# Kernel tuning notes

Hardware: AMD Instinct MI355X
Metric: run time of the kernel (lower is better)

The kernel has to match this reference:

```python
import jax, jax.numpy as jnp
import numpy as np

D = 1024
HS = 64
NH = D // HS


def setup_inputs() -> dict:
    key = jax.random.key(0)
    ks = jax.random.split(key, 8)
    B, S = 2, 2048
    x = jax.random.normal(ks[0], (B, S, D), dtype=jnp.float32)
    y = jax.random.normal(ks[1], (B, S, D), dtype=jnp.float32)
    pad_mask = jax.random.randint(ks[2], (B, S), 0, 2).astype(jnp.int32)
    sc = 1.0 / np.sqrt(D)
    Wq = jax.random.normal(ks[3], (D, D), dtype=jnp.float32) * sc
    Wk = jax.random.normal(ks[4], (D, D), dtype=jnp.float32) * sc
    Wv = jax.random.normal(ks[5], (D, D), dtype=jnp.float32) * sc
    Wp = jax.random.normal(ks[6], (D, D), dtype=jnp.float32) * sc
    bp = jnp.zeros((D,), dtype=jnp.float32)
    return {"x": x, "y": y, "pad_mask": pad_mask, "Wq": Wq, "Wk": Wk, "Wv": Wv, "Wp": Wp, "bp": bp}


def reference(x, y, pad_mask, Wq, Wk, Wv, Wp, bp):
    B, S, _ = x.shape
    # torch Linear: out = in @ W.T  (bias=False for q/k/v)
    q = (y @ Wq.T).reshape(B, S, NH, HS).transpose(0, 2, 1, 3)  # [B,H,S,hs]
    k = (x @ Wk.T).reshape(B, S, NH, HS).transpose(0, 2, 1, 3)
    v = (x @ Wv.T).reshape(B, S, NH, HS).transpose(0, 2, 1, 3)
    att = jnp.einsum('bhqd,bhkd->bhqk', q, k) * (HS ** -0.5)  # [B,H,S,S]
    att = jnp.where((pad_mask == 0)[:, None, None, :], -jnp.inf, att)
    att = jax.nn.softmax(att, axis=-1)
    out = jnp.einsum('bhqk,bhkd->bhqd', att, v)  # [B,H,S,hs]
    out = out.transpose(0, 2, 1, 3).reshape(B, S, D)
    return out @ Wp.T + bp
```

## Files before the change

kernel.cpp:

```cpp
#include <hip/hip_runtime.h>
#include <hip/hip_bf16.h>
#include <stdint.h>

typedef unsigned short u16;
typedef unsigned int u32;
typedef float __attribute__((ext_vector_type(4))) f32x4;
typedef __bf16 __attribute__((ext_vector_type(8))) bfrag;
typedef u16 __attribute__((ext_vector_type(8))) u16x8;

#define DEV static __device__ __forceinline__

DEV u16 f2bf(float f) {
  union { float f; u32 u; } c; c.f = f;
  u32 u = c.u;
  u += 0x7fffu + ((u >> 16) & 1u);
  return (u16)(u >> 16);
}

DEV u16 bf16bits(float f) {
  __hip_bfloat16 h = __float2bfloat16(f);
  return *reinterpret_cast<u16*>(&h);
}

DEV float exp2a(float x) { return __builtin_amdgcn_exp2f(x); }

typedef const u32 __attribute__((address_space(1)))* gas_t;
typedef u32 __attribute__((address_space(3)))* las_t;

DEV void async16(const void* g, void* l) {
  __builtin_amdgcn_global_load_lds((gas_t)(uintptr_t)g, (las_t)(uintptr_t)l, 16, 0, 0);
}

__global__ __launch_bounds__(256) void convert_all(
    const float* __restrict__ x, const float* __restrict__ y,
    const float* __restrict__ wq, const float* __restrict__ wk,
    const float* __restrict__ wv, const float* __restrict__ wp,
    u16* __restrict__ xb, u16* __restrict__ yb,
    u16* __restrict__ wqb, u16* __restrict__ wkb,
    u16* __restrict__ wvb, u16* __restrict__ wpb) {
  const int NX4 = (2 * 2048 * 1024) / 4;
  const int NW4 = (1024 * 1024) / 4;
  const int total = 2 * NX4 + 4 * NW4;
  for (int i = blockIdx.x * blockDim.x + threadIdx.x; i < total;
       i += gridDim.x * blockDim.x) {
    const float4* s; ushort4* d; int off;
    if (i < NX4) { s = (const float4*)x; d = (ushort4*)xb; off = i; }
    else if (i < 2 * NX4) { s = (const float4*)y; d = (ushort4*)yb; off = i - NX4; }
    else {
      int k = i - 2 * NX4; int wsel = k >> 18; off = k & (NW4 - 1);
      s = (const float4*)(wsel == 0 ? wq : wsel == 1 ? wk : wsel == 2 ? wv : wp);
      d = (ushort4*)(wsel == 0 ? wqb : wsel == 1 ? wkb : wsel == 2 ? wvb : wpb);
    }
    float4 v = s[off];
    ushort4 o; o.x = f2bf(v.x); o.y = f2bf(v.y); o.z = f2bf(v.z); o.w = f2bf(v.w);
    d[off] = o;
  }
}

__global__ __launch_bounds__(256, 3) void gemm_qkv(
    const u16* __restrict__ xb, const u16* __restrict__ yb,
    const u16* __restrict__ wqb, const u16* __restrict__ wkb,
    const u16* __restrict__ wvb,
    u16* __restrict__ Qb, u16* __restrict__ Kb2, u16* __restrict__ Vtb) {
  const int Kd = 1024, Nd = 1024;
  __shared__ __align__(16) u16 arena[18432];
  u16* Als = arena;
  u16* Bls = arena + 8192;

  const int gid = blockIdx.x;
  const int seg = gid >> 8;
  const int bb = gid & 255;
  const int m0 = (bb >> 3) * 128, n0 = (bb & 7) * 128;
  const u16* A  = (seg == 0) ? yb : xb;
  const u16* Bw = (seg == 0) ? wqb : (seg == 1 ? wkb : wvb);

  const int t = threadIdx.x;
  const int lane = t & 63, w = t >> 6;
  const int wr = w >> 1, wc = w & 1;
  const int r15 = lane & 15, g = lane >> 4;
  const int rdx = (r15 & 7) << 3;

  const int srow = t >> 3;
  const int scol = ((t & 7) ^ (srow & 7)) * 8;

  f32x4 acc[4][4] = {{}};
  const u16* ga = A + (size_t)(m0 + srow) * Kd + scol;
  const u16* gb = Bw + (size_t)(n0 + srow) * Kd + scol;

  for (int k0 = 0; k0 < Kd; k0 += 64) {
#pragma unroll
    for (int c = 0; c < 4; ++c) {
      async16(ga + (size_t)c * 32 * Kd + k0, &Als[c * 2048 + t * 8]);
      async16(gb + (size_t)c * 32 * Kd + k0, &Bls[c * 2048 + t * 8]);
    }
    __syncthreads();
#pragma unroll
    for (int ks = 0; ks < 2; ++ks) {
      const int cb = (ks * 32 + g * 8) ^ rdx;
      bfrag af[4], bfr[4];
#pragma unroll
      for (int i = 0; i < 4; i++)
        af[i] = *(const bfrag*)&Als[(wr * 64 + i * 16 + r15) * 64 + cb];
#pragma unroll
      for (int j = 0; j < 4; j++)
        bfr[j] = *(const bfrag*)&Bls[(wc * 64 + j * 16 + r15) * 64 + cb];
#pragma unroll
      for (int i = 0; i < 4; i++)
#pragma unroll
        for (int j = 0; j < 4; j++)
          acc[i][j] = __builtin_amdgcn_mfma_f32_16x16x32_bf16(af[i], bfr[j], acc[i][j], 0, 0, 0);
    }
    __syncthreads();
  }

  if (seg < 2) {
    u16* C = (seg == 0) ? Qb : Kb2;
    const float scale = (seg == 0) ? 0.18033688f : 1.0f;
#pragma unroll
    for (int i = 0; i < 4; i++) {
#pragma unroll
      for (int j = 0; j < 4; j++) {
        int col = n0 + wc * 64 + j * 16 + r15;
        int row = m0 + wr * 64 + i * 16 + g * 4;
#pragma unroll
        for (int r = 0; r < 4; r++)
          C[(size_t)(row + r) * Nd + col] = f2bf(acc[i][j][r] * scale);
      }
    }
  } else {
    u16* Tw = arena + w * 4608;
#pragma unroll
    for (int i = 0; i < 4; i++)
#pragma unroll
      for (int j = 0; j < 4; j++)
#pragma unroll
        for (int r = 0; r < 4; r++)
          Tw[(j * 16 + r15) * 72 + (i * 16 + g * 4 + r)] = f2bf(acc[i][j][r]);
#pragma unroll
    for (int it = 0; it < 8; ++it) {
      int slot = lane + it * 64;
      int nl = slot >> 3, sgm = slot & 7;
      int4 vrow = *(const int4*)&Tw[nl * 72 + sgm * 8];
      int col = n0 + wc * 64 + nl;
      int h = col >> 6, hs = col & 63;
      int rowg = m0 + wr * 64 + sgm * 8;
      int b = rowg >> 11, s = rowg & 2047;
      *(int4*)&Vtb[(((size_t)b * 16 + h) * 64 + hs) * 2048 + s] = vrow;
    }
  }
}

__global__ __launch_bounds__(256, 2) void gemm_proj(
    const u16* __restrict__ A, const u16* __restrict__ Bw,
    float* __restrict__ C, const float* __restrict__ bias) {
  const int Kd = 1024, Nd = 1024;
  __shared__ __align__(16) u16 Als[64 * 64];
  __shared__ __align__(16) u16 Bls[128 * 64];
  const int t = threadIdx.x;
  const int lane = t & 63, w = t >> 6;
  const int wr = w >> 1, wc = w & 1;
  const int r15 = lane & 15, g = lane >> 4;
  const int m0 = blockIdx.y * 64, n0 = blockIdx.x * 128;
  const int rdx = (r15 & 7) << 3;
  const int srow = t >> 3;
  const int scol = ((t & 7) ^ (srow & 7)) * 8;

  f32x4 acc[2][4] = {{}};
  const u16* ga = A + (size_t)(m0 + srow) * Kd + scol;
  const u16* gb = Bw + (size_t)(n0 + srow) * Kd + scol;

  for (int k0 = 0; k0 < Kd; k0 += 64) {
#pragma unroll
    for (int c = 0; c < 2; ++c)
      async16(ga + (size_t)c * 32 * Kd + k0, &Als[c * 2048 + t * 8]);
#pragma unroll
    for (int c = 0; c < 4; ++c)
      async16(gb + (size_t)c * 32 * Kd + k0, &Bls[c * 2048 + t * 8]);
    __syncthreads();
#pragma unroll
    for (int ks = 0; ks < 2; ++ks) {
      const int cb = (ks * 32 + g * 8) ^ rdx;
      bfrag af[2], bfr[4];
#pragma unroll
      for (int i = 0; i < 2; i++)
        af[i] = *(const bfrag*)&Als[(wr * 32 + i * 16 + r15) * 64 + cb];
#pragma unroll
      for (int j = 0; j < 4; j++)
        bfr[j] = *(const bfrag*)&Bls[(wc * 64 + j * 16 + r15) * 64 + cb];
#pragma unroll
      for (int i = 0; i < 2; i++)
#pragma unroll
        for (int j = 0; j < 4; j++)
          acc[i][j] = __builtin_amdgcn_mfma_f32_16x16x32_bf16(af[i], bfr[j], acc[i][j], 0, 0, 0);
    }
    __syncthreads();
  }

#pragma unroll
  for (int i = 0; i < 2; i++) {
#pragma unroll
    for (int j = 0; j < 4; j++) {
      int col = n0 + wc * 64 + j * 16 + r15;
      int row = m0 + wr * 32 + i * 16 + g * 4;
      float bv = bias[col];
#pragma unroll
      for (int r = 0; r < 4; r++)
        C[(size_t)(row + r) * Nd + col] = acc[i][j][r] + bv;
    }
  }
}

__global__ __launch_bounds__(256, 2) void attn_fwd(
    const u16* __restrict__ Q, const u16* __restrict__ Kb,
    const u16* __restrict__ Vt, const int* __restrict__ mask,
    u16* __restrict__ O) {
  __shared__ __align__(16) u16 Kls[2][64 * 64];
  __shared__ __align__(16) u16 Vls[2][64 * 64];
  __shared__ __align__(16) u16 Pls[4][32 * 64];
  __shared__ float biasl[2][64];

  const int bid = blockIdx.x;
  const int swz = (bid & 7) * 64 + (bid >> 3);
  const int qblk = swz & 15, bh = swz >> 4;
  const int b = bh >> 4, h = bh & 15;
  const int t = threadIdx.x, lane = t & 63, w = t >> 6;
  const int r15 = lane & 15, g = lane >> 4;
  const int qbase = qblk * 128 + w * 32;

  bfrag aQ[2][2];
  {
    const u16* Qg = Q + ((size_t)b * 2048 + qbase) * 1024 + h * 64;
#pragma unroll
    for (int mf = 0; mf < 2; ++mf)
#pragma unroll
      for (int ks = 0; ks < 2; ++ks)
        aQ[mf][ks] = *(const bfrag*)&Qg[(size_t)(mf * 16 + r15) * 1024 + ks * 32 + g * 8];
  }

  bfrag ones;
  {
    u16x8 ob = {0x3F80, 0x3F80, 0x3F80, 0x3F80, 0x3F80, 0x3F80, 0x3F80, 0x3F80};
    ones = *(bfrag*)&ob;
  }

  f32x4 oacc[2][4] = {};
  f32x4 osum[2] = {};

  const u16* Kg = Kb + (size_t)b * 2048 * 1024 + h * 64;
  const u16* Vg = Vt + (size_t)bh * 64 * 2048;
  const int* mg = mask + b * 2048;

  const int rdx = (r15 & 7) << 3;
  const int srow = t >> 3;
  const int scol = (((t & 7) ^ (srow & 7)) * 8);

  auto stage_async = [&](int kv0, int buf) {
    async16(&Kg[(size_t)(kv0 + srow) * 1024 + scol],        &Kls[buf][t * 8]);
    async16(&Kg[(size_t)(kv0 + 32 + srow) * 1024 + scol],   &Kls[buf][2048 + t * 8]);
    async16(&Vg[(size_t)srow * 2048 + kv0 + scol],          &Vls[buf][t * 8]);
    async16(&Vg[(size_t)(32 + srow) * 2048 + kv0 + scol],   &Vls[buf][2048 + t * 8]);
  };

  stage_async(0, 0);
  if (t < 64) biasl[0][t] = mg[t] ? 0.f : -1e30f;
  __syncthreads();

  float nbias = 0.f;
  for (int kt = 0; kt < 32; ++kt) {
    const int cur = kt & 1;
    if (kt < 31) {
      stage_async((kt + 1) * 64, cur ^ 1);
      if (t < 64) nbias = mg[(kt + 1) * 64 + t] ? 0.f : -1e30f;
    }

    f32x4 sc[2][4] = {};
    __builtin_amdgcn_s_setprio(1);
#pragma unroll
    for (int ks = 0; ks < 2; ++ks) {
      const int cb = (ks * 32 + g * 8) ^ rdx;
#pragma unroll
      for (int nf = 0; nf < 4; ++nf) {
        bfrag bK = *(const bfrag*)&Kls[cur][(nf * 16 + r15) * 64 + cb];
#pragma unroll
        for (int mf = 0; mf < 2; ++mf)
          sc[mf][nf] = __builtin_amdgcn_mfma_f32_16x16x32_bf16(aQ[mf][ks], bK, sc[mf][nf], 0, 0, 0);
      }
    }
    __builtin_amdgcn_s_setprio(0);

    float bcol[4];
#pragma unroll
    for (int nf = 0; nf < 4; ++nf) bcol[nf] = biasl[cur][nf * 16 + r15];

#pragma unroll
    for (int mf = 0; mf < 2; ++mf)
#pragma unroll
      for (int i = 0; i < 4; i++) {
        const int prow = mf * 16 + g * 4 + i;
        const int pxr = (prow & 7) << 3;
        u16* pr = &Pls[w][prow * 64];
#pragma unroll
        for (int nf = 0; nf < 4; ++nf) {
          float p = exp2a(sc[mf][nf][i] + bcol[nf]);
          pr[(nf * 16 + r15) ^ pxr] = bf16bits(p);
        }
      }

    __builtin_amdgcn_s_setprio(1);
#pragma unroll
    for (int ks = 0; ks < 2; ++ks) {
      const int cb = (ks * 32 + g * 8) ^ rdx;
      bfrag aP[2];
#pragma unroll
      for (int mf = 0; mf < 2; ++mf)
        aP[mf] = *(const bfrag*)&Pls[w][(mf * 16 + r15) * 64 + cb];
#pragma unroll
      for (int nf = 0; nf < 4; ++nf) {
        bfrag bV = *(const bfrag*)&Vls[cur][(nf * 16 + r15) * 64 + cb];
#pragma unroll
        for (int mf = 0; mf < 2; ++mf)
          oacc[mf][nf] = __builtin_amdgcn_mfma_f32_16x16x32_bf16(aP[mf], bV, oacc[mf][nf], 0, 0, 0);
      }
#pragma unroll
      for (int mf = 0; mf < 2; ++mf)
        osum[mf] = __builtin_amdgcn_mfma_f32_16x16x32_bf16(aP[mf], ones, osum[mf], 0, 0, 0);
    }
    __builtin_amdgcn_s_setprio(0);

    if (kt < 31 && t < 64) biasl[cur ^ 1][t] = nbias;
    __syncthreads();
  }

  u16* Og = O + ((size_t)b * 2048 + qbase) * 1024 + h * 64;
#pragma unroll
  for (int mf = 0; mf < 2; ++mf)
#pragma unroll
    for (int i = 0; i < 4; i++) {
      float rl = 1.f / osum[mf][i];
      size_t ro = (size_t)(mf * 16 + g * 4 + i) * 1024;
#pragma unroll
      for (int nf = 0; nf < 4; ++nf)
        Og[ro + nf * 16 + r15] = f2bf(oacc[mf][nf][i] * rl);
    }
}

extern "C" void kernel_launch(void* const* d_in, const int* in_sizes, int n_in,
                              void* d_out, int out_size, void* d_ws, size_t ws_size,
                              hipStream_t stream) {
  const float* x  = (const float*)d_in[0];
  const float* y  = (const float*)d_in[1];
  const int*  msk = (const int*)d_in[2];
  const float* Wq = (const float*)d_in[3];
  const float* Wk = (const float*)d_in[4];
  const float* Wv = (const float*)d_in[5];
  const float* Wp = (const float*)d_in[6];
  const float* bp = (const float*)d_in[7];

  char* ws = (char*)d_ws;
  const size_t SZ_XB = (size_t)2 * 2048 * 1024 * 2;
  const size_t SZ_W  = (size_t)1024 * 1024 * 2;
  u16* xb  = (u16*)(ws);
  u16* yb  = (u16*)(ws + SZ_XB);
  u16* wqb = (u16*)(ws + 2 * SZ_XB);
  u16* wkb = (u16*)(ws + 2 * SZ_XB + SZ_W);
  u16* wvb = (u16*)(ws + 2 * SZ_XB + 2 * SZ_W);
  u16* wpb = (u16*)(ws + 2 * SZ_XB + 3 * SZ_W);
  u16* Qb  = (u16*)(ws + 2 * SZ_XB + 4 * SZ_W);
  u16* Kb2 = (u16*)(ws + 3 * SZ_XB + 4 * SZ_W);
  u16* Vtb = (u16*)(ws + 4 * SZ_XB + 4 * SZ_W);
  u16* Ob  = (u16*)(ws + 5 * SZ_XB + 4 * SZ_W);

  convert_all<<<2048, 256, 0, stream>>>(x, y, Wq, Wk, Wv, Wp, xb, yb, wqb, wkb, wvb, wpb);
  gemm_qkv<<<768, 256, 0, stream>>>(xb, yb, wqb, wkb, wvb, Qb, Kb2, Vtb);
  attn_fwd<<<512, 256, 0, stream>>>(Qb, Kb2, Vtb, msk, Ob);
  dim3 gg(8, 64);
  gemm_proj<<<gg, 256, 0, stream>>>(Ob, wpb, (float*)d_out, bp);
}
```

Measured before the change: 117.6 us.

## Split attention KV range across two blocks and merge with a reduce kernel

Adds a split-KV (flash-decoding style) path that gives each attention block half of the key tiles, doubling the grid from 512 to 1024 blocks so more of the GPU's compute units are occupied. Each split writes unnormalized fp32 partial outputs and row sums to workspace, and a new reduce kernel adds them, normalizes, and converts to bf16. The trade is extra global traffic for the fp32 partials (about 32 MB written and read back) plus one more launch. The path is used only when the workspace is large enough, and the row-sum buffer reuses the yb region, which is no longer needed by that point.

```diff
diff --git a/kernel.cpp b/kernel.cpp
--- a/kernel.cpp
+++ b/kernel.cpp
@@ -210,22 +210,27 @@
   }
 }
 
+template <int NSPLIT>
 __global__ __launch_bounds__(256, 2) void attn_fwd(
     const u16* __restrict__ Q, const u16* __restrict__ Kb,
     const u16* __restrict__ Vt, const int* __restrict__ mask,
-    u16* __restrict__ O) {
+    u16* __restrict__ O, float* __restrict__ Op, float* __restrict__ Lp) {
   __shared__ __align__(16) u16 Kls[2][64 * 64];
   __shared__ __align__(16) u16 Vls[2][64 * 64];
   __shared__ __align__(16) u16 Pls[4][32 * 64];
   __shared__ float biasl[2][64];
 
   const int bid = blockIdx.x;
-  const int swz = (bid & 7) * 64 + (bid >> 3);
-  const int qblk = swz & 15, bh = swz >> 4;
+  const int swz = (bid & 7) * (NSPLIT * 64) + (bid >> 3);
+  const int qblk = swz & 15;
+  const int split = (NSPLIT == 2) ? ((swz >> 4) & 1) : 0;
+  const int bh = (NSPLIT == 2) ? (swz >> 5) : (swz >> 4);
   const int b = bh >> 4, h = bh & 15;
   const int t = threadIdx.x, lane = t & 63, w = t >> 6;
   const int r15 = lane & 15, g = lane >> 4;
   const int qbase = qblk * 128 + w * 32;
+  const int ktile0 = split * (32 / NSPLIT);
+  const int NT = 32 / NSPLIT;
 
   bfrag aQ[2][2];
   {
@@ -261,16 +266,17 @@
     async16(&Vg[(size_t)(32 + srow) * 2048 + kv0 + scol],   &Vls[buf][2048 + t * 8]);
   };
 
-  stage_async(0, 0);
-  if (t < 64) biasl[0][t] = mg[t] ? 0.f : -1e30f;
+  stage_async(ktile0 * 64, 0);
+  if (t < 64) biasl[0][t] = mg[ktile0 * 64 + t] ? 0.f : -1e30f;
   __syncthreads();
 
   float nbias = 0.f;
-  for (int kt = 0; kt < 32; ++kt) {
+  for (int kt = 0; kt < NT; ++kt) {
     const int cur = kt & 1;
-    if (kt < 31) {
-      stage_async((kt + 1) * 64, cur ^ 1);
-      if (t < 64) nbias = mg[(kt + 1) * 64 + t] ? 0.f : -1e30f;
+    if (kt < NT - 1) {
+      int nkv = (ktile0 + kt + 1) * 64;
+      stage_async(nkv, cur ^ 1);
+      if (t < 64) nbias = mg[nkv + t] ? 0.f : -1e30f;
     }
 
     f32x4 sc[2][4] = {};
@@ -327,21 +333,58 @@
     }
     __builtin_amdgcn_s_setprio(0);
 
-    if (kt < 31 && t < 64) biasl[cur ^ 1][t] = nbias;
+    if (kt < NT - 1 && t < 64) biasl[cur ^ 1][t] = nbias;
     __syncthreads();
   }
 
-  u16* Og = O + ((size_t)b * 2048 + qbase) * 1024 + h * 64;
-#pragma unroll
-  for (int mf = 0; mf < 2; ++mf)
-#pragma unroll
-    for (int i = 0; i < 4; i++) {
-      float rl = 1.f / osum[mf][i];
-      size_t ro = (size_t)(mf * 16 + g * 4 + i) * 1024;
-#pragma unroll
-      for (int nf = 0; nf < 4; ++nf)
-        Og[ro + nf * 16 + r15] = f2bf(oacc[mf][nf][i] * rl);
-    }
+  if constexpr (NSPLIT == 1) {
+    u16* Og = O + ((size_t)b * 2048 + qbase) * 1024 + h * 64;
+#pragma unroll
+    for (int mf = 0; mf < 2; ++mf)
+#pragma unroll
+      for (int i = 0; i < 4; i++) {
+        float rl = 1.f / osum[mf][i];
+        size_t ro = (size_t)(mf * 16 + g * 4 + i) * 1024;
+#pragma unroll
+        for (int nf = 0; nf < 4; ++nf)
+          Og[ro + nf * 16 + r15] = f2bf(oacc[mf][nf][i] * rl);
+      }
+  } else {
+    float* Og = Op + (size_t)split * 4194304 + ((size_t)b * 2048 + qbase) * 1024 + h * 64;
+    float* Lg = Lp + (size_t)split * 65536 + ((size_t)b * 16 + h) * 2048 + qbase;
+#pragma unroll
+    for (int mf = 0; mf < 2; ++mf)
+#pragma unroll
+      for (int i = 0; i < 4; i++) {
+        size_t ro = (size_t)(mf * 16 + g * 4 + i) * 1024;
+#pragma unroll
+        for (int nf = 0; nf < 4; ++nf)
+          Og[ro + nf * 16 + r15] = oacc[mf][nf][i];
+        if (r15 == 0) Lg[mf * 16 + g * 4 + i] = osum[mf][i];
+      }
+  }
+}
+
+__global__ __launch_bounds__(256) void attn_reduce(
+    const float* __restrict__ Op, const float* __restrict__ Lp,
+    u16* __restrict__ Ob) {
+  int idx = blockIdx.x * 256 + threadIdx.x;
+  int row = idx >> 7;
+  int c8 = (idx & 127) * 8;
+  int h = c8 >> 6;
+  int b = row >> 11, s = row & 2047;
+  int li = (b * 16 + h) * 2048 + s;
+  float rl = 1.f / (Lp[li] + Lp[65536 + li]);
+  const float4* p1 = (const float4*)&Op[(size_t)row * 1024 + c8];
+  const float4* p2 = (const float4*)&Op[4194304 + (size_t)row * 1024 + c8];
+  float4 a0 = p1[0], a1 = p1[1], b0 = p2[0], b1 = p2[1];
+  ushort4 o0, o1;
+  o0.x = f2bf((a0.x + b0.x) * rl); o0.y = f2bf((a0.y + b0.y) * rl);
+  o0.z = f2bf((a0.z + b0.z) * rl); o0.w = f2bf((a0.w + b0.w) * rl);
+  o1.x = f2bf((a1.x + b1.x) * rl); o1.y = f2bf((a1.y + b1.y) * rl);
+  o1.z = f2bf((a1.z + b1.z) * rl); o1.w = f2bf((a1.w + b1.w) * rl);
+  *(ushort4*)&Ob[(size_t)idx * 8] = o0;
+  *(ushort4*)&Ob[(size_t)idx * 8 + 4] = o1;
 }
 
 extern "C" void kernel_launch(void* const* d_in, const int* in_sizes, int n_in,
@@ -369,10 +412,19 @@
   u16* Kb2 = (u16*)(ws + 3 * SZ_XB + 4 * SZ_W);
   u16* Vtb = (u16*)(ws + 4 * SZ_XB + 4 * SZ_W);
   u16* Ob  = (u16*)(ws + 5 * SZ_XB + 4 * SZ_W);
+  float* Lp = (float*)(ws + 2 * SZ_XB);
+  const size_t OFF_OP = 6 * SZ_XB + 4 * SZ_W;
+  const size_t NEED = OFF_OP + (size_t)2 * 4194304 * 4;
 
   convert_all<<<2048, 256, 0, stream>>>(x, y, Wq, Wk, Wv, Wp, xb, yb, wqb, wkb, wvb, wpb);
   gemm_qkv<<<768, 256, 0, stream>>>(xb, yb, wqb, wkb, wvb, Qb, Kb2, Vtb);
-  attn_fwd<<<512, 256, 0, stream>>>(Qb, Kb2, Vtb, msk, Ob);
+  if (ws_size >= NEED) {
+    float* Op = (float*)(ws + OFF_OP);
+    attn_fwd<2><<<1024, 256, 0, stream>>>(Qb, Kb2, Vtb, msk, nullptr, Op, Lp);
+    attn_reduce<<<2048, 256, 0, stream>>>(Op, Lp, Ob);
+  } else {
+    attn_fwd<1><<<512, 256, 0, stream>>>(Qb, Kb2, Vtb, msk, Ob, nullptr, nullptr);
+  }
   dim3 gg(8, 64);
   gemm_proj<<<gg, 256, 0, stream>>>(Ob, wpb, (float*)d_out, bp);
 }
```

New measurement: 128.2 us. 1.09x slower.
